# Kernel optimization log

Hardware: AMD Instinct MI355X
Metric: run time of the kernel (lower is better)

Reference implementation:

```python
import jax, jax.numpy as jnp
import numpy as np

N_CLASSES = 1000  # init kwarg n_classes
BIG = 1e24        # diagonal fill used by get_center_distances


def setup_inputs() -> dict:
    key = jax.random.key(0)
    k1, k2 = jax.random.split(key)
    embeddings = jax.random.normal(k1, (400000, 64), dtype=jnp.float32)
    target = jax.random.randint(k2, (400000,), 0, N_CLASSES)
    return {"embeddings": embeddings, "target": target}


def reference(embeddings, target):
    # Training-mode IILoss forward (returned loss does not depend on running buffers).
    n = embeddings.shape[0]
    ones = jnp.ones((n,), embeddings.dtype)
    counts = jax.ops.segment_sum(ones, target, num_segments=N_CLASSES)          # [C]
    sums = jax.ops.segment_sum(embeddings, target, num_segments=N_CLASSES)      # [C, D]
    mu = sums / jnp.maximum(counts, 1.0)[:, None]                                # per-class mean

    # intra_spread = sum_i ||e_i - mu[target_i]||^2 / n  (single fused pass)
    diff = embeddings - mu[target]
    intra_spread = jnp.sum(diff * diff) / n

    # pairwise squared distances between centers of classes present in the batch
    sq = jnp.sum(mu * mu, axis=1)                                                # [C]
    dists = sq[:, None] + sq[None, :] - 2.0 * (mu @ mu.T)                        # [C, C]
    present = counts > 0
    mask = present[:, None] & present[None, :] & ~jnp.eye(N_CLASSES, dtype=bool)
    dists = jnp.where(mask, dists, jnp.asarray(BIG, dists.dtype))
    inter_separation = -jnp.min(dists)
    return (intra_spread, inter_separation)
```

## Files before the change

kernel.cpp:

```cpp
#include <hip/hip_runtime.h>

#define NCLS 1000
#define DIM 64
#define CURW 32
#define SPLIT 8
#define STAGE 512
#define CAP 1024
#define TPB 256
#define TILE 32
#define NTA 32
#define NPAIR (NTA * (NTA + 1) / 2)

struct Ws {
    unsigned minkey;
    unsigned pad_[31];
    int      cur[NCLS * CURW];
    float    mu[NCLS * DIM];
    float    sq[NCLS];
    float    part[NCLS * SPLIT * DIM];
    float    part_ssq[NCLS * SPLIT];
    float    cls_ssq[NCLS];
    float    cls_mt[NCLS];
};

struct RedSm  { int sidx[STAGE]; float facc[4][DIM]; float fssq[4]; };
struct PairSm { float As[TILE][DIM + 1]; float Bs[TILE][DIM + 1];
                float sqa[TILE], sqb[TILE]; int pa[TILE], pb[TILE];
                unsigned redm[4]; };
struct FinSm  { double sd[TPB], md[TPB]; };

__device__ __forceinline__ unsigned fkey(float x) {
    unsigned b = __float_as_uint(x);
    return (b & 0x80000000u) ? ~b : (b | 0x80000000u);
}
__device__ __forceinline__ float funkey(unsigned k) {
    return (k & 0x80000000u) ? __uint_as_float(k & 0x7FFFFFFFu)
                             : __uint_as_float(~k);
}

__global__ __launch_bounds__(TPB) void f_zero(Ws* ws) {
    const int gtid = blockIdx.x * TPB + threadIdx.x;
    if (gtid < NCLS) ws->cur[gtid * CURW] = 0;
    if (gtid == 0) ws->minkey = fkey(1.0e24f);
}

__global__ __launch_bounds__(TPB) void f_scatter(const int* __restrict__ tgt, int n,
                                                 Ws* ws, int* __restrict__ bucket) {
    for (int r = blockIdx.x * TPB + threadIdx.x; r < n; r += (int)gridDim.x * TPB) {
        const int c = tgt[r];
        const int p = atomicAdd(&ws->cur[c * CURW], 1);
        if (p < CAP) bucket[c * CAP + p] = r;
    }
}

__global__ __launch_bounds__(TPB) void f_reduce(const float* __restrict__ emb,
                                                const int* __restrict__ bucket,
                                                Ws* __restrict__ ws) {
    __shared__ RedSm sm;
    const int vb   = blockIdx.x;
    const int c    = vb / SPLIT;
    const int sp   = vb % SPLIT;
    const int t    = threadIdx.x;
    const int lane = t & 63;
    const int w    = t >> 6;
    const int cnt  = min(ws->cur[c * CURW], CAP);
    const int i0   = (cnt * sp) / SPLIT;
    const int i1   = (cnt * (sp + 1)) / SPLIT;
    const int base = c * CAP + i0;
    const int m    = i1 - i0;

    float acc = 0.f, ssq = 0.f;
    for (int s0 = 0; s0 < m; s0 += STAGE) {
        const int mm = min(STAGE, m - s0);
        __syncthreads();
        for (int i = t; i < mm; i += TPB) sm.sidx[i] = bucket[base + s0 + i];
        __syncthreads();
        int p = w;
        for (; p + 28 < mm; p += 32) {
            const int r0 = sm.sidx[p];      const int r1 = sm.sidx[p + 4];
            const int r2 = sm.sidx[p + 8];  const int r3 = sm.sidx[p + 12];
            const int r4 = sm.sidx[p + 16]; const int r5 = sm.sidx[p + 20];
            const int r6 = sm.sidx[p + 24]; const int r7 = sm.sidx[p + 28];
            const float v0 = emb[(size_t)r0 * DIM + lane];
            const float v1 = emb[(size_t)r1 * DIM + lane];
            const float v2 = emb[(size_t)r2 * DIM + lane];
            const float v3 = emb[(size_t)r3 * DIM + lane];
            const float v4 = emb[(size_t)r4 * DIM + lane];
            const float v5 = emb[(size_t)r5 * DIM + lane];
            const float v6 = emb[(size_t)r6 * DIM + lane];
            const float v7 = emb[(size_t)r7 * DIM + lane];
            acc += v0 + v1 + v2 + v3 + v4 + v5 + v6 + v7;
            ssq += v0 * v0 + v1 * v1 + v2 * v2 + v3 * v3
                 + v4 * v4 + v5 * v5 + v6 * v6 + v7 * v7;
        }
        for (; p + 12 < mm; p += 16) {
            const int r0 = sm.sidx[p];      const int r1 = sm.sidx[p + 4];
            const int r2 = sm.sidx[p + 8];  const int r3 = sm.sidx[p + 12];
            const float v0 = emb[(size_t)r0 * DIM + lane];
            const float v1 = emb[(size_t)r1 * DIM + lane];
            const float v2 = emb[(size_t)r2 * DIM + lane];
            const float v3 = emb[(size_t)r3 * DIM + lane];
            acc += v0 + v1 + v2 + v3;
            ssq += v0 * v0 + v1 * v1 + v2 * v2 + v3 * v3;
        }
        for (; p < mm; p += 4) {
            const float v0 = emb[(size_t)sm.sidx[p] * DIM + lane];
            acc += v0;
            ssq += v0 * v0;
        }
    }
    __syncthreads();
    sm.facc[w][lane] = acc;
    float s = ssq;
    for (int o = 32; o; o >>= 1) s += __shfl_down(s, o);
    if (lane == 0) sm.fssq[w] = s;
    __syncthreads();
    if (t < DIM)
        ws->part[vb * DIM + t] = sm.facc[0][t] + sm.facc[1][t]
                               + sm.facc[2][t] + sm.facc[3][t];
    if (t == 0)
        ws->part_ssq[vb] = sm.fssq[0] + sm.fssq[1] + sm.fssq[2] + sm.fssq[3];
}

__global__ __launch_bounds__(TPB) void f_centers(Ws* ws) {
    const int c    = blockIdx.x * 4 + (threadIdx.x >> 6);
    const int lane = threadIdx.x & 63;
    if (c >= NCLS) return;
    const int cnt = min(ws->cur[c * CURW], CAP);
    float v = 0.f;
    #pragma unroll
    for (int s2 = 0; s2 < SPLIT; ++s2) v += ws->part[(c * SPLIT + s2) * DIM + lane];
    const float m = v / (float)max(cnt, 1);
    ws->mu[c * DIM + lane] = m;
    float p = m * m;
    for (int o = 32; o; o >>= 1) p += __shfl_down(p, o);
    if (lane == 0) {
        ws->sq[c]     = p;
        ws->cls_mt[c] = cnt ? (float)cnt * p : 0.f;
        float q = 0.f;
        #pragma unroll
        for (int s2 = 0; s2 < SPLIT; ++s2) q += ws->part_ssq[c * SPLIT + s2];
        ws->cls_ssq[c] = q;
    }
}

__global__ __launch_bounds__(TPB) void f_pairs(Ws* ws) {
    __shared__ PairSm sm;
    const int t = threadIdx.x;
    int rem = blockIdx.x, ta = 0;
    while (rem >= NTA - ta) { rem -= NTA - ta; ++ta; }
    const int tb = ta + rem;

    for (int i = t; i < TILE * (DIM / 4); i += TPB) {
        const int r = i >> 4, c4 = (i & 15) * 4;
        const int ga = ta * TILE + r;
        const int gb = tb * TILE + r;
        float4 va = make_float4(0.f, 0.f, 0.f, 0.f);
        float4 vb = make_float4(0.f, 0.f, 0.f, 0.f);
        if (ga < NCLS) va = *reinterpret_cast<const float4*>(&ws->mu[ga * DIM + c4]);
        if (gb < NCLS) vb = *reinterpret_cast<const float4*>(&ws->mu[gb * DIM + c4]);
        sm.As[r][c4 + 0] = va.x; sm.As[r][c4 + 1] = va.y;
        sm.As[r][c4 + 2] = va.z; sm.As[r][c4 + 3] = va.w;
        sm.Bs[r][c4 + 0] = vb.x; sm.Bs[r][c4 + 1] = vb.y;
        sm.Bs[r][c4 + 2] = vb.z; sm.Bs[r][c4 + 3] = vb.w;
    }
    if (t < TILE) {
        const int ga = ta * TILE + t;
        sm.pa[t]  = (ga < NCLS) ? (min(ws->cur[ga * CURW], CAP) > 0) : 0;
        sm.sqa[t] = (ga < NCLS) ? ws->sq[ga] : 0.f;
    } else if (t < 2 * TILE) {
        const int tt = t - TILE;
        const int gb = tb * TILE + tt;
        sm.pb[tt]  = (gb < NCLS) ? (min(ws->cur[gb * CURW], CAP) > 0) : 0;
        sm.sqb[tt] = (gb < NCLS) ? ws->sq[gb] : 0.f;
    }
    __syncthreads();

    const int ty2 = (t >> 4) * 2;
    const int tx2 = (t & 15) * 2;
    float dot[2][2] = {{0.f, 0.f}, {0.f, 0.f}};
    #pragma unroll 8
    for (int k = 0; k < DIM; ++k) {
        float av[2], bv[2];
        av[0] = sm.As[ty2][k];     av[1] = sm.As[ty2 + 1][k];
        bv[0] = sm.Bs[tx2][k];     bv[1] = sm.Bs[tx2 + 1][k];
        dot[0][0] += av[0] * bv[0]; dot[0][1] += av[0] * bv[1];
        dot[1][0] += av[1] * bv[0]; dot[1][1] += av[1] * bv[1];
    }

    float best = 3.0e38f;
    #pragma unroll
    for (int i = 0; i < 2; ++i) {
        #pragma unroll
        for (int j = 0; j < 2; ++j) {
            const int ga = ta * TILE + ty2 + i;
            const int gb = tb * TILE + tx2 + j;
            const bool valid = sm.pa[ty2 + i] && sm.pb[tx2 + j] && (ga != gb);
            const float dd = sm.sqa[ty2 + i] + sm.sqb[tx2 + j] - 2.f * dot[i][j];
            if (valid) best = fminf(best, dd);
        }
    }
    for (int o = 32; o; o >>= 1) best = fminf(best, __shfl_down(best, o));
    if ((t & 63) == 0) sm.redm[t >> 6] = fkey(best);
    __syncthreads();
    if (t == 0) {
        unsigned mk = sm.redm[0];
        #pragma unroll
        for (int q = 1; q < 4; ++q) mk = min(mk, sm.redm[q]);
        atomicMin(&ws->minkey, mk);
    }
}

__global__ __launch_bounds__(TPB) void f_final(const Ws* ws, float* out, int n) {
    __shared__ FinSm sm;
    const int t = threadIdx.x;
    double a = 0.0, b = 0.0;
    for (int i = t; i < NCLS; i += TPB) { a += (double)ws->cls_ssq[i]; b += (double)ws->cls_mt[i]; }
    sm.sd[t] = a; sm.md[t] = b;
    __syncthreads();
    for (int s = 128; s >= 1; s >>= 1) {
        if (t < s) { sm.sd[t] += sm.sd[t + s]; sm.md[t] += sm.md[t + s]; }
        __syncthreads();
    }
    if (t == 0) {
        out[0] = (float)((sm.sd[0] - sm.md[0]) / (double)n);
        out[1] = -funkey(ws->minkey);
    }
}

extern "C" void kernel_launch(void* const* d_in, const int* in_sizes, int n_in,
                              void* d_out, int out_size, void* d_ws, size_t ws_size,
                              hipStream_t stream) {
    const float* emb = (const float*)d_in[0];
    const int*   tgt = (const int*)d_in[1];
    float* out = (float*)d_out;
    const int n = in_sizes[1];
    Ws* ws = (Ws*)d_ws;
    int* bucket = (int*)((char*)d_ws + sizeof(Ws));

    f_zero   <<<(NCLS + TPB - 1) / TPB, TPB, 0, stream>>>(ws);
    f_scatter<<<1024, TPB, 0, stream>>>(tgt, n, ws, bucket);
    f_reduce <<<NCLS * SPLIT, TPB, 0, stream>>>(emb, bucket, ws);
    f_centers<<<NCLS / 4, TPB, 0, stream>>>(ws);
    f_pairs  <<<NPAIR, TPB, 0, stream>>>(ws);
    f_final  <<<1, TPB, 0, stream>>>(ws, out, n);
}
```

Baseline: 65.64 us.

## Shard per-class bucket counters by block group to cut atomic contention

The scatter pass now spreads each class across 8 sub-buckets, chosen by the low bits of the block index, each with its own counter and a 128-slot capacity. This replaces one hot atomic counter per class. Each reduce block handles exactly one sub-bucket instead of slicing a per-class bucket. The centers kernel sums the sub-bucket counts and stores a per-class count for the pair kernel. The goal is less atomic serialization in the scatter. The cost is more counters to zero and a risk of overflow if class sizes become skewed, since each group can hold only 128 rows.

After: 65.27 us. No clear change (-0.6%).

```diff
diff --git a/kernel.cpp b/kernel.cpp
--- a/kernel.cpp
+++ b/kernel.cpp
@@ -2,10 +2,10 @@
 
 #define NCLS 1000
 #define DIM 64
+#define NG 8
+#define CAPG 128
 #define CURW 32
-#define SPLIT 8
 #define STAGE 512
-#define CAP 1024
 #define TPB 256
 #define TILE 32
 #define NTA 32
@@ -14,11 +14,12 @@
 struct Ws {
     unsigned minkey;
     unsigned pad_[31];
-    int      cur[NCLS * CURW];
+    int      cur[NCLS * NG * CURW];
+    int      cls_cnt[NCLS];
     float    mu[NCLS * DIM];
     float    sq[NCLS];
-    float    part[NCLS * SPLIT * DIM];
-    float    part_ssq[NCLS * SPLIT];
+    float    part[NCLS * NG * DIM];
+    float    part_ssq[NCLS * NG];
     float    cls_ssq[NCLS];
     float    cls_mt[NCLS];
 };
@@ -40,16 +41,18 @@
 
 __global__ __launch_bounds__(TPB) void f_zero(Ws* ws) {
     const int gtid = blockIdx.x * TPB + threadIdx.x;
-    if (gtid < NCLS) ws->cur[gtid * CURW] = 0;
+    if (gtid < NCLS * NG) ws->cur[gtid * CURW] = 0;
     if (gtid == 0) ws->minkey = fkey(1.0e24f);
 }
 
 __global__ __launch_bounds__(TPB) void f_scatter(const int* __restrict__ tgt, int n,
                                                  Ws* ws, int* __restrict__ bucket) {
+    const int g = blockIdx.x & (NG - 1);
     for (int r = blockIdx.x * TPB + threadIdx.x; r < n; r += (int)gridDim.x * TPB) {
-        const int c = tgt[r];
-        const int p = atomicAdd(&ws->cur[c * CURW], 1);
-        if (p < CAP) bucket[c * CAP + p] = r;
+        const int c  = tgt[r];
+        const int cg = c * NG + g;
+        const int p  = atomicAdd(&ws->cur[cg * CURW], 1);
+        if (p < CAPG) bucket[cg * CAPG + p] = r;
     }
 }
 
@@ -58,16 +61,11 @@
                                                 Ws* __restrict__ ws) {
     __shared__ RedSm sm;
     const int vb   = blockIdx.x;
-    const int c    = vb / SPLIT;
-    const int sp   = vb % SPLIT;
     const int t    = threadIdx.x;
     const int lane = t & 63;
     const int w    = t >> 6;
-    const int cnt  = min(ws->cur[c * CURW], CAP);
-    const int i0   = (cnt * sp) / SPLIT;
-    const int i1   = (cnt * (sp + 1)) / SPLIT;
-    const int base = c * CAP + i0;
-    const int m    = i1 - i0;
+    const int m    = min(ws->cur[vb * CURW], CAPG);
+    const int base = vb * CAPG;
 
     float acc = 0.f, ssq = 0.f;
     for (int s0 = 0; s0 < m; s0 += STAGE) {
@@ -126,20 +124,23 @@
     const int c    = blockIdx.x * 4 + (threadIdx.x >> 6);
     const int lane = threadIdx.x & 63;
     if (c >= NCLS) return;
-    const int cnt = min(ws->cur[c * CURW], CAP);
+    int cnt = 0;
+    #pragma unroll
+    for (int g = 0; g < NG; ++g) cnt += min(ws->cur[(c * NG + g) * CURW], CAPG);
     float v = 0.f;
     #pragma unroll
-    for (int s2 = 0; s2 < SPLIT; ++s2) v += ws->part[(c * SPLIT + s2) * DIM + lane];
+    for (int g = 0; g < NG; ++g) v += ws->part[(c * NG + g) * DIM + lane];
     const float m = v / (float)max(cnt, 1);
     ws->mu[c * DIM + lane] = m;
     float p = m * m;
     for (int o = 32; o; o >>= 1) p += __shfl_down(p, o);
     if (lane == 0) {
-        ws->sq[c]     = p;
-        ws->cls_mt[c] = cnt ? (float)cnt * p : 0.f;
+        ws->cls_cnt[c] = cnt;
+        ws->sq[c]      = p;
+        ws->cls_mt[c]  = cnt ? (float)cnt * p : 0.f;
         float q = 0.f;
         #pragma unroll
-        for (int s2 = 0; s2 < SPLIT; ++s2) q += ws->part_ssq[c * SPLIT + s2];
+        for (int g = 0; g < NG; ++g) q += ws->part_ssq[c * NG + g];
         ws->cls_ssq[c] = q;
     }
 }
@@ -166,12 +167,12 @@
     }
     if (t < TILE) {
         const int ga = ta * TILE + t;
-        sm.pa[t]  = (ga < NCLS) ? (min(ws->cur[ga * CURW], CAP) > 0) : 0;
+        sm.pa[t]  = (ga < NCLS) ? (ws->cls_cnt[ga] > 0) : 0;
         sm.sqa[t] = (ga < NCLS) ? ws->sq[ga] : 0.f;
     } else if (t < 2 * TILE) {
         const int tt = t - TILE;
         const int gb = tb * TILE + tt;
-        sm.pb[tt]  = (gb < NCLS) ? (min(ws->cur[gb * CURW], CAP) > 0) : 0;
+        sm.pb[tt]  = (gb < NCLS) ? (ws->cls_cnt[gb] > 0) : 0;
         sm.sqb[tt] = (gb < NCLS) ? ws->sq[gb] : 0.f;
     }
     __syncthreads();
@@ -238,9 +239,9 @@
     Ws* ws = (Ws*)d_ws;
     int* bucket = (int*)((char*)d_ws + sizeof(Ws));
 
-    f_zero   <<<(NCLS + TPB - 1) / TPB, TPB, 0, stream>>>(ws);
+    f_zero   <<<(NCLS * NG + TPB - 1) / TPB, TPB, 0, stream>>>(ws);
     f_scatter<<<1024, TPB, 0, stream>>>(tgt, n, ws, bucket);
-    f_reduce <<<NCLS * SPLIT, TPB, 0, stream>>>(emb, bucket, ws);
+    f_reduce <<<NCLS * NG, TPB, 0, stream>>>(emb, bucket, ws);
     f_centers<<<NCLS / 4, TPB, 0, stream>>>(ws);
     f_pairs  <<<NPAIR, TPB, 0, stream>>>(ws);
     f_final  <<<1, TPB, 0, stream>>>(ws, out, n);
```
